# Optimization experiments

Hardware: AMD Instinct MI355X
Metric: run time of the kernel (lower is better)

## Reference

```python
import jax, jax.numpy as jnp
import numpy as np

EPS = 1e-7  # entropy eps
DIAG_EPS = 1e-8
LEAK = 0.2  # LeakyReLU slope


def _entropy(p):
    # EntropyLoss: mean over leading dims of -sum(p*log(p+eps), -1)
    return jnp.mean(-jnp.sum(p * jnp.log(p + EPS), axis=-1))


def setup_inputs() -> dict:
    key = jax.random.key(0)
    ks = jax.random.split(key, 7)
    B, S, C, F, E, H = 256, 6, 80, 2048, 300, 1024
    x = jax.random.normal(ks[0], (B, F, 14, 14), dtype=jnp.float32)
    inp = jax.random.normal(ks[1], (C, E), dtype=jnp.float32) * 0.1
    y = (jax.random.uniform(ks[2], (B, C)) < 0.1).astype(jnp.float32)
    # persistent co-occurrence buffer (non-negative counts)
    comatrix = jax.random.uniform(ks[3], (S, C, C), dtype=jnp.float32) * 50.0
    W_scene = jax.random.normal(ks[4], (F, S), dtype=jnp.float32) * 0.02
    W1 = jax.random.uniform(ks[5], (E, H), dtype=jnp.float32, minval=-1, maxval=1) / np.sqrt(H)
    W2 = jax.random.uniform(ks[6], (H, F), dtype=jnp.float32, minval=-1, maxval=1) / np.sqrt(F)
    return {"x": x, "inp": inp, "y": y, "comatrix": comatrix,
            "W_scene": W_scene, "W1": W1, "W2": W2}


def reference(x, inp, y, comatrix, W_scene, W1, W2):
    B = x.shape[0]
    S, C, _ = comatrix.shape
    # backbone output -> MaxPool2d(14,14) == global max over the 14x14 map
    img_feats = jnp.max(x, axis=(2, 3))                       # [B, F]
    scene_scores = img_feats @ W_scene                        # [B, S]
    scene_probs = jax.nn.softmax(scene_scores, axis=-1)
    # --- training-path comatrix scatter update (comat_smooth=False) ---
    batch_comats = y[:, :, None] * y[:, None, :]              # [B, C, C]
    ids = jnp.argmax(scene_probs, axis=-1)                    # [B]
    comatrix = comatrix + jnp.zeros_like(comatrix).at[ids].add(batch_comats)
    # --- entropy terms ---
    sample_en = _entropy(scene_probs)
    max_en = _entropy(jnp.full((S,), 1.0 / S, dtype=scene_probs.dtype))
    batch_en = (max_en - _entropy(jnp.mean(scene_probs, axis=0))) * 100.0
    # --- comatrix2prob: row-normalize by diagonal, force diag=1 ---
    diag = jnp.diagonal(comatrix, axis1=1, axis2=2)[:, :, None]  # [S, C, 1]
    comat = comatrix / (diag + DIAG_EPS)
    eye = jnp.eye(C, dtype=comat.dtype)
    comat = comat * (1.0 - eye) + eye
    comats = comat[ids]                                       # gather [B, C, C]
    # --- gen_adj: adj = D^{-1/2} A^T D^{-1/2}, D = rowsums(A) ---
    D = jax.lax.rsqrt(jnp.sum(comats, axis=2))                # [B, C]
    adjs = D[:, :, None] * jnp.swapaxes(comats, 1, 2) * D[:, None, :]
    # --- 2-layer GCN ---
    h = adjs @ (inp @ W1)                                     # [B, C, 1024]
    h = jnp.where(h > 0, h, LEAK * h)
    h = adjs @ (h @ W2)                                       # [B, C, 2048]
    output = jnp.einsum('bcf,bf->bc', h, img_feats)           # [B, C]
    return (output, scene_probs, sample_en, batch_en, comats)
```

## Files before the change

### kernel.cpp

```cpp
#include <hip/hip_runtime.h>
#include <math.h>

#define B_ 256
#define S_ 6
#define C_ 80
#define F_ 2048
#define E_ 300
#define H_ 1024
#define EPS_ 1e-7f
#define DEPS_ 1e-8f
#define LEAK_ 0.2f

#define IMG_OFF   0u
#define Z_OFF     524288u
#define COMAT_OFF 606208u
#define ADJA_OFF  644608u
#define G_OFF     683008u
#define PART_OFF  1174528u
#define IDS_OFF   5368832u
#define MP_OFF    5369088u
#define SEN_OFF   5369094u

#define OUT0_OFF 0
#define PROB_OFF 20480
#define SEN_OUT  22016
#define BEN_OUT  22017
#define CMTS_OFF 22018

__global__ __launch_bounds__(256) void k_maxpool(const float* __restrict__ x,
                                                 float* __restrict__ img) {
    int pair = blockIdx.x * 4 + (threadIdx.x >> 6);
    int lane = threadIdx.x & 63;
    const float4* xp = (const float4*)x + (size_t)pair * 49;
    float m = -INFINITY;
    if (lane < 49) {
        float4 v = xp[lane];
        m = fmaxf(fmaxf(v.x, v.y), fmaxf(v.z, v.w));
    }
#pragma unroll
    for (int off = 32; off >= 1; off >>= 1) m = fmaxf(m, __shfl_xor(m, off));
    if (lane == 0) img[pair] = m;
}

__global__ __launch_bounds__(256) void k_scene(const float* __restrict__ img,
                                               const float* __restrict__ Ws,
                                               float* __restrict__ probs_out,
                                               int* __restrict__ ids,
                                               float* __restrict__ mp,
                                               float* __restrict__ sen) {
    __shared__ float red[6][256];
    int b = blockIdx.x, tid = threadIdx.x;
    float acc[6] = {0, 0, 0, 0, 0, 0};
#pragma unroll
    for (int i = 0; i < 8; i++) {
        int f = tid + i * 256;
        float a = img[b * F_ + f];
#pragma unroll
        for (int s = 0; s < 6; s++) acc[s] += a * Ws[f * 6 + s];
    }
    for (int s = 0; s < 6; s++) red[s][tid] = acc[s];
    __syncthreads();
    for (int off = 128; off > 0; off >>= 1) {
        if (tid < off)
            for (int s = 0; s < 6; s++) red[s][tid] += red[s][tid + off];
        __syncthreads();
    }
    if (tid == 0) {
        float sc[6], mx = -INFINITY;
        for (int s = 0; s < 6; s++) { sc[s] = red[s][0]; mx = fmaxf(mx, sc[s]); }
        float sum = 0.f;
        for (int s = 0; s < 6; s++) { sc[s] = expf(sc[s] - mx); sum += sc[s]; }
        float inv = 1.0f / sum;
        float p[6], ent = 0.f;
        int best = 0; float bv = -1.f;
        for (int s = 0; s < 6; s++) {
            p[s] = sc[s] * inv;
            probs_out[b * 6 + s] = p[s];
            ent -= p[s] * logf(p[s] + EPS_);
            if (p[s] > bv) { bv = p[s]; best = s; }
            atomicAdd(&mp[s], p[s]);
        }
        atomicAdd(sen, ent);
        ids[b] = best;
    }
}

__global__ __launch_bounds__(256) void k_comat(const float* __restrict__ y,
                                               const float* __restrict__ cm_in,
                                               const int* __restrict__ ids,
                                               float* __restrict__ comat,
                                               float* __restrict__ adjA) {
    int s = blockIdx.x, tid = threadIdx.x;
    __shared__ unsigned long long colq[80][4];
    __shared__ float cm[6400];
    __shared__ float diag[80], Dn[80];
    __shared__ int idsL[256];
    idsL[tid] = ids[tid];
    __syncthreads();
    int wave = tid >> 6, lane = tid & 63;
    int b = tid;
    bool ok = (idsL[b] == s);
    for (int i = 0; i < 80; i++) {
        bool pred = ok && (y[b * 80 + i] != 0.0f);
        unsigned long long mk = __ballot(pred);
        if (lane == 0) colq[i][wave] = mk;
    }
    __syncthreads();
    for (int p = tid; p < 6400; p += 256) {
        int i = p / 80, j = p - i * 80;
        int cnt = 0;
#pragma unroll
        for (int w = 0; w < 4; w++) cnt += __popcll(colq[i][w] & colq[j][w]);
        cm[p] = cm_in[s * 6400 + p] + (float)cnt;
    }
    __syncthreads();
    if (tid < 80) diag[tid] = cm[tid * 81];
    __syncthreads();
    for (int p = tid; p < 6400; p += 256) {
        int i = p / 80, j = p - i * 80;
        float v = (i == j) ? 1.0f : cm[p] / (diag[i] + DEPS_);
        cm[p] = v;
        comat[s * 6400 + p] = v;
    }
    __syncthreads();
    if (tid < 80) {
        float rs = 0.f;
        for (int j = 0; j < 80; j++) rs += cm[tid * 80 + j];
        Dn[tid] = 1.0f / sqrtf(rs);
    }
    __syncthreads();
    for (int p = tid; p < 6400; p += 256) {
        int i = p / 80, j = p - i * 80;
        adjA[s * 6400 + p] = Dn[i] * cm[j * 80 + i] * Dn[j];
    }
}

__global__ __launch_bounds__(256) void k_z(const float* __restrict__ inp,
                                           const float* __restrict__ W1,
                                           float* __restrict__ Z) {
    int c = blockIdx.x >> 2;
    int h = ((blockIdx.x & 3) << 8) + threadIdx.x;
    float acc = 0.f;
    for (int e = 0; e < E_; e++) acc += inp[c * E_ + e] * W1[e * H_ + h];
    Z[c * H_ + h] = acc;
}

__global__ __launch_bounds__(256) void k_g(const float* __restrict__ adjA,
                                           const float* __restrict__ Z,
                                           float* __restrict__ g) {
    int s = blockIdx.x / 80, c = blockIdx.x % 80;
    const float* row = adjA + (s * 80 + c) * 80;
    const float4* Z4 = (const float4*)Z;
    float4 acc = {0, 0, 0, 0};
    for (int j = 0; j < 80; j++) {
        float a = row[j];
        float4 z = Z4[j * 256 + threadIdx.x];
        acc.x += a * z.x; acc.y += a * z.y; acc.z += a * z.z; acc.w += a * z.w;
    }
    acc.x = acc.x > 0.f ? acc.x : LEAK_ * acc.x;
    acc.y = acc.y > 0.f ? acc.y : LEAK_ * acc.y;
    acc.z = acc.z > 0.f ? acc.z : LEAK_ * acc.z;
    acc.w = acc.w > 0.f ? acc.w : LEAK_ * acc.w;
    ((float4*)g)[(s * 80 + c) * 256 + threadIdx.x] = acc;
}

__global__ __launch_bounds__(256) void k_ugemm(const float* __restrict__ A,
                                               const float* __restrict__ Bm,
                                               float* __restrict__ part) {
    __shared__ float As[16 * 132];
    __shared__ float Bs[16 * 132];
    int tid = threadIdx.x;
    int m0 = blockIdx.y * 128, h0 = blockIdx.x * 128;
    int kbase = blockIdx.z * 128;
    float acc[8][8];
#pragma unroll
    for (int i = 0; i < 8; i++)
#pragma unroll
        for (int j = 0; j < 8; j++) acc[i][j] = 0.f;
    int r0 = (tid >> 4) << 3, c0 = (tid & 15) << 3;
    for (int st = 0; st < 8; st++) {
        int kc = kbase + st * 16;
#pragma unroll
        for (int l = 0; l < 2; l++) {
            int fid = tid + (l << 8);
            int r = fid >> 2, kq = fid & 3;
            float4 av = *(const float4*)(A + (size_t)(m0 + r) * 2048 + kc + (kq << 2));
            float4 bv = *(const float4*)(Bm + (size_t)(h0 + r) * 2048 + kc + (kq << 2));
            int kk = kq << 2;
            As[(kk + 0) * 132 + r] = av.x; As[(kk + 1) * 132 + r] = av.y;
            As[(kk + 2) * 132 + r] = av.z; As[(kk + 3) * 132 + r] = av.w;
            Bs[(kk + 0) * 132 + r] = bv.x; Bs[(kk + 1) * 132 + r] = bv.y;
            Bs[(kk + 2) * 132 + r] = bv.z; Bs[(kk + 3) * 132 + r] = bv.w;
        }
        __syncthreads();
#pragma unroll
        for (int k = 0; k < 16; k++) {
            float4 a0 = *(const float4*)&As[k * 132 + r0];
            float4 a1 = *(const float4*)&As[k * 132 + r0 + 4];
            float4 b0 = *(const float4*)&Bs[k * 132 + c0];
            float4 b1 = *(const float4*)&Bs[k * 132 + c0 + 4];
            float ar[8] = {a0.x, a0.y, a0.z, a0.w, a1.x, a1.y, a1.z, a1.w};
            float br[8] = {b0.x, b0.y, b0.z, b0.w, b1.x, b1.y, b1.z, b1.w};
#pragma unroll
            for (int i = 0; i < 8; i++)
#pragma unroll
                for (int j = 0; j < 8; j++) acc[i][j] += ar[i] * br[j];
        }
        __syncthreads();
    }
    float* pu = part + (size_t)blockIdx.z * 262144;
#pragma unroll
    for (int i = 0; i < 8; i++) {
        int row = m0 + r0 + i;
        float4 v0 = {acc[i][0], acc[i][1], acc[i][2], acc[i][3]};
        float4 v1 = {acc[i][4], acc[i][5], acc[i][6], acc[i][7]};
        *(float4*)(pu + (size_t)row * 1024 + h0 + c0) = v0;
        *(float4*)(pu + (size_t)row * 1024 + h0 + c0 + 4) = v1;
    }
}

__global__ __launch_bounds__(320) void k_out(const float* __restrict__ part,
                                             const float* __restrict__ g,
                                             const float* __restrict__ adjA,
                                             const int* __restrict__ ids,
                                             float* __restrict__ out0) {
    __shared__ float ul[1024];
    __shared__ float tp[320];
    __shared__ float tv[80];
    int b = blockIdx.x, tid = threadIdx.x;
    int s = ids[b];
    for (int h = tid; h < 1024; h += 320) {
        float a = 0.f;
#pragma unroll
        for (int z = 0; z < 16; z++) a += part[z * 262144 + b * 1024 + h];
        ul[h] = a;
    }
    __syncthreads();
    int c = tid >> 2, q = tid & 3;
    const float4* gp = (const float4*)(g + (s * 80 + c) * 1024 + q * 256);
    const float4* up = (const float4*)(ul + q * 256);
    float a = 0.f;
    for (int k = 0; k < 64; k++) {
        float4 gv = gp[k];
        float4 uv = up[k];
        a += gv.x * uv.x + gv.y * uv.y + gv.z * uv.z + gv.w * uv.w;
    }
    tp[tid] = a;
    __syncthreads();
    if (tid < 80) tv[tid] = tp[tid * 4] + tp[tid * 4 + 1] + tp[tid * 4 + 2] + tp[tid * 4 + 3];
    __syncthreads();
    if (tid < 80) {
        const float* ar = adjA + (s * 80 + tid) * 80;
        float o = 0.f;
        for (int j = 0; j < 80; j++) o += ar[j] * tv[j];
        out0[b * 80 + tid] = o;
    }
}

__global__ __launch_bounds__(256) void k_gather(const float* __restrict__ comat,
                                                const int* __restrict__ ids,
                                                float* __restrict__ cmts) {
    int b = blockIdx.x;
    int s = ids[b];
    const float2* src = (const float2*)(comat + s * 6400);
    float2* dst = (float2*)(cmts + (size_t)b * 6400);
    for (int i = threadIdx.x; i < 3200; i += 256) dst[i] = src[i];
}

__global__ void k_final(const float* __restrict__ mp, const float* __restrict__ sen,
                        float* __restrict__ o_sen, float* __restrict__ o_ben) {
    if (threadIdx.x == 0 && blockIdx.x == 0) {
        *o_sen = *sen / 256.0f;
        float ent = 0.f;
        for (int s = 0; s < 6; s++) {
            float q = mp[s] / 256.0f;
            ent -= q * logf(q + EPS_);
        }
        float invS = 1.0f / 6.0f;
        float men = -6.0f * (invS * logf(invS + EPS_));
        *o_ben = (men - ent) * 100.0f;
    }
}

extern "C" void kernel_launch(void* const* d_in, const int* in_sizes, int n_in,
                              void* d_out, int out_size, void* d_ws, size_t ws_size,
                              hipStream_t stream) {
    const float* x    = (const float*)d_in[0];
    const float* inp  = (const float*)d_in[1];
    const float* y    = (const float*)d_in[2];
    const float* cmin = (const float*)d_in[3];
    const float* Ws   = (const float*)d_in[4];
    const float* W1   = (const float*)d_in[5];
    const float* W2   = (const float*)d_in[6];
    float* out = (float*)d_out;
    float* W = (float*)d_ws;

    float* img   = W + IMG_OFF;
    float* Z     = W + Z_OFF;
    float* comat = W + COMAT_OFF;
    float* adjA  = W + ADJA_OFF;
    float* g     = W + G_OFF;
    float* part  = W + PART_OFF;
    int*   ids   = (int*)(W + IDS_OFF);
    float* mp    = W + MP_OFF;
    float* sen   = W + SEN_OFF;

    hipMemsetAsync(mp, 0, 7 * sizeof(float), stream);
    k_maxpool<<<131072, 256, 0, stream>>>(x, img);
    k_scene<<<256, 256, 0, stream>>>(img, Ws, out + PROB_OFF, ids, mp, sen);
    k_comat<<<6, 256, 0, stream>>>(y, cmin, ids, comat, adjA);
    k_z<<<320, 256, 0, stream>>>(inp, W1, Z);
    k_g<<<480, 256, 0, stream>>>(adjA, Z, g);
    k_ugemm<<<dim3(8, 2, 16), 256, 0, stream>>>(img, W2, part);
    k_out<<<256, 320, 0, stream>>>(part, g, adjA, ids, out + OUT0_OFF);
    k_gather<<<256, 256, 0, stream>>>(comat, ids, out + CMTS_OFF);
    k_final<<<1, 64, 0, stream>>>(mp, sen, out + SEN_OUT, out + BEN_OUT);
}
```

Measured before the change: 671.7 us.

## Merge independent kernels into combined launches and drop atomics/memset

Pairs independent stages into single launches by branching on block index: Z projection with maxpool, scene softmax with the W2 GEMM, the g computation with the comat gather, and the output stage with the entropy finalization. The entropy reductions move from global atomics plus a memset into one extra block that reads the stored probabilities and reduces them with wave shuffles. This removes several kernel launches, one memset and the atomics. In exchange, mixed-role grids can load-balance unevenly, and the combined GEMM/scene kernel carries the GEMM's register and shared-memory footprint for all its blocks.

```diff
diff --git a/kernel.cpp b/kernel.cpp
--- a/kernel.cpp
+++ b/kernel.cpp
@@ -18,8 +18,6 @@
 #define G_OFF     683008u
 #define PART_OFF  1174528u
 #define IDS_OFF   5368832u
-#define MP_OFF    5369088u
-#define SEN_OFF   5369094u
 
 #define OUT0_OFF 0
 #define PROB_OFF 20480
@@ -27,61 +25,124 @@
 #define BEN_OUT  22017
 #define CMTS_OFF 22018
 
-__global__ __launch_bounds__(256) void k_maxpool(const float* __restrict__ x,
-                                                 float* __restrict__ img) {
-    int pair = blockIdx.x * 4 + (threadIdx.x >> 6);
-    int lane = threadIdx.x & 63;
-    const float4* xp = (const float4*)x + (size_t)pair * 49;
-    float m = -INFINITY;
-    if (lane < 49) {
-        float4 v = xp[lane];
-        m = fmaxf(fmaxf(v.x, v.y), fmaxf(v.z, v.w));
-    }
-#pragma unroll
-    for (int off = 32; off >= 1; off >>= 1) m = fmaxf(m, __shfl_xor(m, off));
-    if (lane == 0) img[pair] = m;
-}
-
-__global__ __launch_bounds__(256) void k_scene(const float* __restrict__ img,
-                                               const float* __restrict__ Ws,
-                                               float* __restrict__ probs_out,
-                                               int* __restrict__ ids,
-                                               float* __restrict__ mp,
-                                               float* __restrict__ sen) {
-    __shared__ float red[6][256];
-    int b = blockIdx.x, tid = threadIdx.x;
-    float acc[6] = {0, 0, 0, 0, 0, 0};
-#pragma unroll
-    for (int i = 0; i < 8; i++) {
-        int f = tid + i * 256;
-        float a = img[b * F_ + f];
-#pragma unroll
-        for (int s = 0; s < 6; s++) acc[s] += a * Ws[f * 6 + s];
-    }
-    for (int s = 0; s < 6; s++) red[s][tid] = acc[s];
-    __syncthreads();
-    for (int off = 128; off > 0; off >>= 1) {
-        if (tid < off)
-            for (int s = 0; s < 6; s++) red[s][tid] += red[s][tid + off];
+__global__ __launch_bounds__(256) void k_pool_z(const float* __restrict__ x,
+                                                float* __restrict__ img,
+                                                const float* __restrict__ inp,
+                                                const float* __restrict__ W1,
+                                                float* __restrict__ Z) {
+    if (blockIdx.x < 320) {
+        int c = blockIdx.x >> 2;
+        int h = ((blockIdx.x & 3) << 8) + threadIdx.x;
+        float acc = 0.f;
+        for (int e = 0; e < E_; e++) acc += inp[c * E_ + e] * W1[e * H_ + h];
+        Z[c * H_ + h] = acc;
+    } else {
+        int pair = (blockIdx.x - 320) * 4 + (threadIdx.x >> 6);
+        int lane = threadIdx.x & 63;
+        const float4* xp = (const float4*)x + (size_t)pair * 49;
+        float m = -INFINITY;
+        if (lane < 49) {
+            float4 v = xp[lane];
+            m = fmaxf(fmaxf(v.x, v.y), fmaxf(v.z, v.w));
+        }
+#pragma unroll
+        for (int off = 32; off >= 1; off >>= 1) m = fmaxf(m, __shfl_xor(m, off));
+        if (lane == 0) img[pair] = m;
+    }
+}
+
+__global__ __launch_bounds__(256) void k_scene_ugemm(const float* __restrict__ img,
+                                                     const float* __restrict__ Ws,
+                                                     const float* __restrict__ W2,
+                                                     float* __restrict__ probs_out,
+                                                     int* __restrict__ ids,
+                                                     float* __restrict__ part) {
+    __shared__ float sm[2 * 16 * 132];
+    int tid = threadIdx.x;
+    if (blockIdx.x < 256) {
+        float (*red)[256] = (float(*)[256])sm;
+        int b = blockIdx.x;
+        float acc[6] = {0, 0, 0, 0, 0, 0};
+#pragma unroll
+        for (int i = 0; i < 8; i++) {
+            int f = tid + i * 256;
+            float a = img[b * F_ + f];
+#pragma unroll
+            for (int s = 0; s < 6; s++) acc[s] += a * Ws[f * 6 + s];
+        }
+        for (int s = 0; s < 6; s++) red[s][tid] = acc[s];
         __syncthreads();
-    }
-    if (tid == 0) {
-        float sc[6], mx = -INFINITY;
-        for (int s = 0; s < 6; s++) { sc[s] = red[s][0]; mx = fmaxf(mx, sc[s]); }
-        float sum = 0.f;
-        for (int s = 0; s < 6; s++) { sc[s] = expf(sc[s] - mx); sum += sc[s]; }
-        float inv = 1.0f / sum;
-        float p[6], ent = 0.f;
-        int best = 0; float bv = -1.f;
-        for (int s = 0; s < 6; s++) {
-            p[s] = sc[s] * inv;
-            probs_out[b * 6 + s] = p[s];
-            ent -= p[s] * logf(p[s] + EPS_);
-            if (p[s] > bv) { bv = p[s]; best = s; }
-            atomicAdd(&mp[s], p[s]);
-        }
-        atomicAdd(sen, ent);
-        ids[b] = best;
+        for (int off = 128; off > 0; off >>= 1) {
+            if (tid < off)
+                for (int s = 0; s < 6; s++) red[s][tid] += red[s][tid + off];
+            __syncthreads();
+        }
+        if (tid == 0) {
+            float sc[6], mx = -INFINITY;
+            for (int s = 0; s < 6; s++) { sc[s] = red[s][0]; mx = fmaxf(mx, sc[s]); }
+            float sum = 0.f;
+            for (int s = 0; s < 6; s++) { sc[s] = expf(sc[s] - mx); sum += sc[s]; }
+            float inv = 1.0f / sum;
+            int best = 0; float bv = -1.f;
+            for (int s = 0; s < 6; s++) {
+                float p = sc[s] * inv;
+                probs_out[b * 6 + s] = p;
+                if (p > bv) { bv = p; best = s; }
+            }
+            ids[b] = best;
+        }
+    } else {
+        float* As = sm;
+        float* Bs = sm + 16 * 132;
+        int t = blockIdx.x - 256;
+        int bx = t & 7, by = (t >> 3) & 1, bz = t >> 4;
+        int m0 = by * 128, h0 = bx * 128;
+        int kbase = bz * 128;
+        float acc[8][8];
+#pragma unroll
+        for (int i = 0; i < 8; i++)
+#pragma unroll
+            for (int j = 0; j < 8; j++) acc[i][j] = 0.f;
+        int r0 = (tid >> 4) << 3, c0 = (tid & 15) << 3;
+        for (int st = 0; st < 8; st++) {
+            int kc = kbase + st * 16;
+#pragma unroll
+            for (int l = 0; l < 2; l++) {
+                int fid = tid + (l << 8);
+                int r = fid >> 2, kq = fid & 3;
+                float4 av = *(const float4*)(img + (size_t)(m0 + r) * 2048 + kc + (kq << 2));
+                float4 bv = *(const float4*)(W2 + (size_t)(h0 + r) * 2048 + kc + (kq << 2));
+                int kk = kq << 2;
+                As[(kk + 0) * 132 + r] = av.x; As[(kk + 1) * 132 + r] = av.y;
+                As[(kk + 2) * 132 + r] = av.z; As[(kk + 3) * 132 + r] = av.w;
+                Bs[(kk + 0) * 132 + r] = bv.x; Bs[(kk + 1) * 132 + r] = bv.y;
+                Bs[(kk + 2) * 132 + r] = bv.z; Bs[(kk + 3) * 132 + r] = bv.w;
+            }
+            __syncthreads();
+#pragma unroll
+            for (int k = 0; k < 16; k++) {
+                float4 a0 = *(const float4*)&As[k * 132 + r0];
+                float4 a1 = *(const float4*)&As[k * 132 + r0 + 4];
+                float4 b0 = *(const float4*)&Bs[k * 132 + c0];
+                float4 b1 = *(const float4*)&Bs[k * 132 + c0 + 4];
+                float ar[8] = {a0.x, a0.y, a0.z, a0.w, a1.x, a1.y, a1.z, a1.w};
+                float br[8] = {b0.x, b0.y, b0.z, b0.w, b1.x, b1.y, b1.z, b1.w};
+#pragma unroll
+                for (int i = 0; i < 8; i++)
+#pragma unroll
+                    for (int j = 0; j < 8; j++) acc[i][j] += ar[i] * br[j];
+            }
+            __syncthreads();
+        }
+        float* pu = part + (size_t)bz * 262144;
+#pragma unroll
+        for (int i = 0; i < 8; i++) {
+            int row = m0 + r0 + i;
+            float4 v0 = {acc[i][0], acc[i][1], acc[i][2], acc[i][3]};
+            float4 v1 = {acc[i][4], acc[i][5], acc[i][6], acc[i][7]};
+            *(float4*)(pu + (size_t)row * 1024 + h0 + c0) = v0;
+            *(float4*)(pu + (size_t)row * 1024 + h0 + c0 + 4) = v1;
+        }
     }
 }
 
@@ -135,99 +196,82 @@
     }
 }
 
-__global__ __launch_bounds__(256) void k_z(const float* __restrict__ inp,
-                                           const float* __restrict__ W1,
-                                           float* __restrict__ Z) {
-    int c = blockIdx.x >> 2;
-    int h = ((blockIdx.x & 3) << 8) + threadIdx.x;
-    float acc = 0.f;
-    for (int e = 0; e < E_; e++) acc += inp[c * E_ + e] * W1[e * H_ + h];
-    Z[c * H_ + h] = acc;
-}
-
-__global__ __launch_bounds__(256) void k_g(const float* __restrict__ adjA,
-                                           const float* __restrict__ Z,
-                                           float* __restrict__ g) {
-    int s = blockIdx.x / 80, c = blockIdx.x % 80;
-    const float* row = adjA + (s * 80 + c) * 80;
-    const float4* Z4 = (const float4*)Z;
-    float4 acc = {0, 0, 0, 0};
-    for (int j = 0; j < 80; j++) {
-        float a = row[j];
-        float4 z = Z4[j * 256 + threadIdx.x];
-        acc.x += a * z.x; acc.y += a * z.y; acc.z += a * z.z; acc.w += a * z.w;
-    }
-    acc.x = acc.x > 0.f ? acc.x : LEAK_ * acc.x;
-    acc.y = acc.y > 0.f ? acc.y : LEAK_ * acc.y;
-    acc.z = acc.z > 0.f ? acc.z : LEAK_ * acc.z;
-    acc.w = acc.w > 0.f ? acc.w : LEAK_ * acc.w;
-    ((float4*)g)[(s * 80 + c) * 256 + threadIdx.x] = acc;
-}
-
-__global__ __launch_bounds__(256) void k_ugemm(const float* __restrict__ A,
-                                               const float* __restrict__ Bm,
-                                               float* __restrict__ part) {
-    __shared__ float As[16 * 132];
-    __shared__ float Bs[16 * 132];
-    int tid = threadIdx.x;
-    int m0 = blockIdx.y * 128, h0 = blockIdx.x * 128;
-    int kbase = blockIdx.z * 128;
-    float acc[8][8];
-#pragma unroll
-    for (int i = 0; i < 8; i++)
-#pragma unroll
-        for (int j = 0; j < 8; j++) acc[i][j] = 0.f;
-    int r0 = (tid >> 4) << 3, c0 = (tid & 15) << 3;
-    for (int st = 0; st < 8; st++) {
-        int kc = kbase + st * 16;
-#pragma unroll
-        for (int l = 0; l < 2; l++) {
-            int fid = tid + (l << 8);
-            int r = fid >> 2, kq = fid & 3;
-            float4 av = *(const float4*)(A + (size_t)(m0 + r) * 2048 + kc + (kq << 2));
-            float4 bv = *(const float4*)(Bm + (size_t)(h0 + r) * 2048 + kc + (kq << 2));
-            int kk = kq << 2;
-            As[(kk + 0) * 132 + r] = av.x; As[(kk + 1) * 132 + r] = av.y;
-            As[(kk + 2) * 132 + r] = av.z; As[(kk + 3) * 132 + r] = av.w;
-            Bs[(kk + 0) * 132 + r] = bv.x; Bs[(kk + 1) * 132 + r] = bv.y;
-            Bs[(kk + 2) * 132 + r] = bv.z; Bs[(kk + 3) * 132 + r] = bv.w;
-        }
-        __syncthreads();
-#pragma unroll
-        for (int k = 0; k < 16; k++) {
-            float4 a0 = *(const float4*)&As[k * 132 + r0];
-            float4 a1 = *(const float4*)&As[k * 132 + r0 + 4];
-            float4 b0 = *(const float4*)&Bs[k * 132 + c0];
-            float4 b1 = *(const float4*)&Bs[k * 132 + c0 + 4];
-            float ar[8] = {a0.x, a0.y, a0.z, a0.w, a1.x, a1.y, a1.z, a1.w};
-            float br[8] = {b0.x, b0.y, b0.z, b0.w, b1.x, b1.y, b1.z, b1.w};
-#pragma unroll
-            for (int i = 0; i < 8; i++)
-#pragma unroll
-                for (int j = 0; j < 8; j++) acc[i][j] += ar[i] * br[j];
-        }
-        __syncthreads();
-    }
-    float* pu = part + (size_t)blockIdx.z * 262144;
-#pragma unroll
-    for (int i = 0; i < 8; i++) {
-        int row = m0 + r0 + i;
-        float4 v0 = {acc[i][0], acc[i][1], acc[i][2], acc[i][3]};
-        float4 v1 = {acc[i][4], acc[i][5], acc[i][6], acc[i][7]};
-        *(float4*)(pu + (size_t)row * 1024 + h0 + c0) = v0;
-        *(float4*)(pu + (size_t)row * 1024 + h0 + c0 + 4) = v1;
-    }
-}
-
-__global__ __launch_bounds__(320) void k_out(const float* __restrict__ part,
-                                             const float* __restrict__ g,
-                                             const float* __restrict__ adjA,
-                                             const int* __restrict__ ids,
-                                             float* __restrict__ out0) {
+__global__ __launch_bounds__(256) void k_g_gather(const float* __restrict__ adjA,
+                                                  const float* __restrict__ Z,
+                                                  float* __restrict__ g,
+                                                  const float* __restrict__ comat,
+                                                  const int* __restrict__ ids,
+                                                  float* __restrict__ cmts) {
+    if (blockIdx.x < 480) {
+        int s = blockIdx.x / 80, c = blockIdx.x % 80;
+        const float* row = adjA + (s * 80 + c) * 80;
+        const float4* Z4 = (const float4*)Z;
+        float4 acc = {0, 0, 0, 0};
+        for (int j = 0; j < 80; j++) {
+            float a = row[j];
+            float4 z = Z4[j * 256 + threadIdx.x];
+            acc.x += a * z.x; acc.y += a * z.y; acc.z += a * z.z; acc.w += a * z.w;
+        }
+        acc.x = acc.x > 0.f ? acc.x : LEAK_ * acc.x;
+        acc.y = acc.y > 0.f ? acc.y : LEAK_ * acc.y;
+        acc.z = acc.z > 0.f ? acc.z : LEAK_ * acc.z;
+        acc.w = acc.w > 0.f ? acc.w : LEAK_ * acc.w;
+        ((float4*)g)[(s * 80 + c) * 256 + threadIdx.x] = acc;
+    } else {
+        int b = blockIdx.x - 480;
+        int s = ids[b];
+        const float2* src = (const float2*)(comat + s * 6400);
+        float2* dst = (float2*)(cmts + (size_t)b * 6400);
+        for (int i = threadIdx.x; i < 3200; i += 256) dst[i] = src[i];
+    }
+}
+
+__global__ __launch_bounds__(320) void k_out_final(const float* __restrict__ part,
+                                                   const float* __restrict__ g,
+                                                   const float* __restrict__ adjA,
+                                                   const int* __restrict__ ids,
+                                                   const float* __restrict__ probs,
+                                                   float* __restrict__ out0,
+                                                   float* __restrict__ o_sen,
+                                                   float* __restrict__ o_ben) {
     __shared__ float ul[1024];
     __shared__ float tp[320];
     __shared__ float tv[80];
-    int b = blockIdx.x, tid = threadIdx.x;
+    int tid = threadIdx.x;
+    if (blockIdx.x == 256) {
+        if (tid < 64) {
+            float lent = 0.f;
+            float lp[6] = {0, 0, 0, 0, 0, 0};
+            for (int i = 0; i < 4; i++) {
+                int b = tid * 4 + i;
+#pragma unroll
+                for (int s = 0; s < 6; s++) {
+                    float p = probs[b * 6 + s];
+                    lp[s] += p;
+                    lent -= p * logf(p + EPS_);
+                }
+            }
+#pragma unroll
+            for (int off = 32; off >= 1; off >>= 1) {
+                lent += __shfl_xor(lent, off);
+#pragma unroll
+                for (int s = 0; s < 6; s++) lp[s] += __shfl_xor(lp[s], off);
+            }
+            if (tid == 0) {
+                *o_sen = lent / 256.0f;
+                float ent = 0.f;
+                for (int s = 0; s < 6; s++) {
+                    float q = lp[s] / 256.0f;
+                    ent -= q * logf(q + EPS_);
+                }
+                float invS = 1.0f / 6.0f;
+                float men = -6.0f * (invS * logf(invS + EPS_));
+                *o_ben = (men - ent) * 100.0f;
+            }
+        }
+        return;
+    }
+    int b = blockIdx.x;
     int s = ids[b];
     for (int h = tid; h < 1024; h += 320) {
         float a = 0.f;
@@ -254,31 +298,6 @@
         float o = 0.f;
         for (int j = 0; j < 80; j++) o += ar[j] * tv[j];
         out0[b * 80 + tid] = o;
-    }
-}
-
-__global__ __launch_bounds__(256) void k_gather(const float* __restrict__ comat,
-                                                const int* __restrict__ ids,
-                                                float* __restrict__ cmts) {
-    int b = blockIdx.x;
-    int s = ids[b];
-    const float2* src = (const float2*)(comat + s * 6400);
-    float2* dst = (float2*)(cmts + (size_t)b * 6400);
-    for (int i = threadIdx.x; i < 3200; i += 256) dst[i] = src[i];
-}
-
-__global__ void k_final(const float* __restrict__ mp, const float* __restrict__ sen,
-                        float* __restrict__ o_sen, float* __restrict__ o_ben) {
-    if (threadIdx.x == 0 && blockIdx.x == 0) {
-        *o_sen = *sen / 256.0f;
-        float ent = 0.f;
-        for (int s = 0; s < 6; s++) {
-            float q = mp[s] / 256.0f;
-            ent -= q * logf(q + EPS_);
-        }
-        float invS = 1.0f / 6.0f;
-        float men = -6.0f * (invS * logf(invS + EPS_));
-        *o_ben = (men - ent) * 100.0f;
     }
 }
 
@@ -302,17 +321,11 @@
     float* g     = W + G_OFF;
     float* part  = W + PART_OFF;
     int*   ids   = (int*)(W + IDS_OFF);
-    float* mp    = W + MP_OFF;
-    float* sen   = W + SEN_OFF;
-
-    hipMemsetAsync(mp, 0, 7 * sizeof(float), stream);
-    k_maxpool<<<131072, 256, 0, stream>>>(x, img);
-    k_scene<<<256, 256, 0, stream>>>(img, Ws, out + PROB_OFF, ids, mp, sen);
+
+    k_pool_z<<<131392, 256, 0, stream>>>(x, img, inp, W1, Z);
+    k_scene_ugemm<<<512, 256, 0, stream>>>(img, Ws, W2, out + PROB_OFF, ids, part);
     k_comat<<<6, 256, 0, stream>>>(y, cmin, ids, comat, adjA);
-    k_z<<<320, 256, 0, stream>>>(inp, W1, Z);
-    k_g<<<480, 256, 0, stream>>>(adjA, Z, g);
-    k_ugemm<<<dim3(8, 2, 16), 256, 0, stream>>>(img, W2, part);
-    k_out<<<256, 320, 0, stream>>>(part, g, adjA, ids, out + OUT0_OFF);
-    k_gather<<<256, 256, 0, stream>>>(comat, ids, out + CMTS_OFF);
-    k_final<<<1, 64, 0, stream>>>(mp, sen, out + SEN_OUT, out + BEN_OUT);
-}
+    k_g_gather<<<736, 256, 0, stream>>>(adjA, Z, g, comat, ids, out + CMTS_OFF);
+    k_out_final<<<257, 320, 0, stream>>>(part, g, adjA, ids, out + PROB_OFF,
+                                         out + OUT0_OFF, out + SEN_OUT, out + BEN_OUT);
+}
```

Result: faster. 626.8 us (-6.7%).
